# Kernel tuning notes

Hardware: AMD Instinct MI355X
Metric: run time of the kernel (lower is better)

## Reference

```python
import jax, jax.numpy as jnp
import numpy as np
import math

B, S, D, H = 2, 2048, 1024, 16
DK = D // H


def setup_inputs() -> dict:
    key = jax.random.key(0)
    ks = jax.random.split(key, 12)
    s = 0.02
    return {
        "query": jax.random.normal(ks[0], (B, S, D), jnp.float32),
        "key": jax.random.normal(ks[1], (B, S, D), jnp.float32),
        "value": jax.random.normal(ks[2], (B, S, D), jnp.float32),
        "mask": jnp.zeros((1, 1, S, S), jnp.float32),
        "Wq": jax.random.normal(ks[3], (D, D), jnp.float32) * s,
        "bq": jnp.zeros((D,), jnp.float32),
        "Wk": jax.random.normal(ks[4], (D, D), jnp.float32) * s,
        "bk": jnp.zeros((D,), jnp.float32),
        "Wv": jax.random.normal(ks[5], (D, D), jnp.float32) * s,
        "bv": jnp.zeros((D,), jnp.float32),
        "Wpost": jax.random.normal(ks[6], (D, D), jnp.float32) * s,
        "bpost": jnp.zeros((D,), jnp.float32),
        "per_dim_scale": jnp.zeros((DK,), jnp.float32),
    }


def reference(query, key, value, mask, Wq, bq, Wk, bk, Wv, bv, Wpost, bpost, per_dim_scale):
    # Linear projections (torch Linear: x @ W.T + b), split heads -> [B, H, S, DK]
    def proj(x, W, b):
        return (x @ W.T + b).reshape(B, S, H, DK).transpose(0, 2, 1, 3)

    q = proj(query, Wq, bq)
    k = proj(key, Wk, bk)
    v = proj(value, Wv, bv)

    # PerDimScale: scale = (1/ln2) / sqrt(d_k) * softplus(per_dim_scale)
    r_softplus_0 = 1.442695041
    scale = (r_softplus_0 / math.sqrt(DK)) * jax.nn.softplus(per_dim_scale)
    q = q * scale  # broadcast over last dim

    # Full attention matrix [B, H, S, S] + additive mask + softmax (dropout p=0)
    attn = jnp.einsum('bhqd,bhkd->bhqk', q, k) + mask
    attn = jax.nn.softmax(attn, axis=-1)

    out = jnp.einsum('bhqk,bhkd->bhqd', attn, v)
    out = out.transpose(0, 2, 1, 3).reshape(B, S, D)
    return out @ Wpost.T + bpost
```

## Files before the change

kernel.cpp:

```cpp
#include <hip/hip_runtime.h>
#include <math.h>

typedef __bf16 bf16;
typedef __bf16 bf16x8 __attribute__((ext_vector_type(8)));
typedef float f32x4 __attribute__((ext_vector_type(4)));

static constexpr int NB = 2, NS = 2048, ND = 1024, NH = 16, NDK = 64;
static constexpr float LOG2E = 1.442695041f;

__device__ __forceinline__ f32x4 mfma16(bf16x8 a, bf16x8 b, f32x4 c) {
  return __builtin_amdgcn_mfma_f32_16x16x32_bf16(a, b, c, 0, 0, 0);
}

__device__ __forceinline__ float exp2_fast(float x) {
  return __builtin_amdgcn_exp2f(x);
}

__device__ __forceinline__ void gload16(const void* g, void* l) {
  __builtin_amdgcn_global_load_lds(
      (const __attribute__((address_space(1))) void*)g,
      (__attribute__((address_space(3))) void*)l, 16, 0, 0);
}

__global__ void prep_kernel(const float* __restrict__ pds, float* __restrict__ scale,
                            const float* __restrict__ mask, int* __restrict__ flag, int n4) {
  if (blockIdx.x == 256) {
    int i = threadIdx.x;
    if (i < NDK) {
      float x = pds[i];
      float sp = fmaxf(x, 0.0f) + log1pf(expf(-fabsf(x)));
      scale[i] = (LOG2E * LOG2E / 8.0f) * sp;
    }
    return;
  }
  int idx = blockIdx.x * blockDim.x + threadIdx.x;
  int stride = 256 * blockDim.x;
  unsigned acc = 0;
  for (int i = idx; i < n4; i += stride) {
    float4 v = ((const float4*)mask)[i];
    acc |= (__float_as_uint(v.x) << 1) | (__float_as_uint(v.y) << 1)
         | (__float_as_uint(v.z) << 1) | (__float_as_uint(v.w) << 1);
  }
  if (acc != 0) atomicOr(flag, 1);
}

__global__ __launch_bounds__(256) void cvt_bf16(
    const float* __restrict__ s0, const float* __restrict__ s1, const float* __restrict__ s2,
    const float* __restrict__ s3, const float* __restrict__ s4, const float* __restrict__ s5,
    const float* __restrict__ s6,
    bf16* __restrict__ d0, bf16* __restrict__ d1, bf16* __restrict__ d2,
    bf16* __restrict__ d3, bf16* __restrict__ d4, bf16* __restrict__ d5,
    bf16* __restrict__ d6, int n8x, int n8w) {
  const int y = blockIdx.y;
  const float* s = y == 0 ? s0 : y == 1 ? s1 : y == 2 ? s2 : y == 3 ? s3
                 : y == 4 ? s4 : y == 5 ? s5 : s6;
  bf16* d = y == 0 ? d0 : y == 1 ? d1 : y == 2 ? d2 : y == 3 ? d3
          : y == 4 ? d4 : y == 5 ? d5 : d6;
  const int n8 = y < 3 ? n8x : n8w;
  for (int i = blockIdx.x * 256 + threadIdx.x; i < n8; i += gridDim.x * 256) {
    const float4* f = (const float4*)s + 2 * (size_t)i;
    float4 a = f[0], b = f[1];
    bf16x8 o;
    o[0] = (bf16)a.x; o[1] = (bf16)a.y; o[2] = (bf16)a.z; o[3] = (bf16)a.w;
    o[4] = (bf16)b.x; o[5] = (bf16)b.y; o[6] = (bf16)b.z; o[7] = (bf16)b.w;
    *((bf16x8*)d + i) = o;
  }
}

__global__ __launch_bounds__(256) void qkv_mm(
    const bf16* __restrict__ Xq, const bf16* __restrict__ Xk, const bf16* __restrict__ Xv,
    const bf16* __restrict__ Wqb, const bf16* __restrict__ Wkb, const bf16* __restrict__ Wvb,
    const float* __restrict__ bq, const float* __restrict__ bk, const float* __restrict__ bv,
    const float* __restrict__ scale2,
    bf16* __restrict__ Qs, bf16* __restrict__ Ks, bf16* __restrict__ Vt, int mode0) {
  __shared__ __align__(16) bf16 la[128 * 64];
  __shared__ __align__(16) bf16 lb[128 * 64];
  const int which = mode0 + blockIdx.y;
  const bf16* A  = which == 0 ? Xq  : which == 1 ? Xk  : Wvb;
  const bf16* Bm = which == 0 ? Wqb : which == 1 ? Wkb : Xv;
  const int t = threadIdx.x, lane = t & 63, wave = t >> 6;
  const int wm = wave >> 1, wn = wave & 1;
  int bm, bn;
  if (which == 2) { bm = blockIdx.x & 7; bn = blockIdx.x >> 3; }
  else            { bm = blockIdx.x >> 3; bn = blockIdx.x & 7; }
  const int g = lane >> 4, l15 = lane & 15;
  const int sr = wave * 8 + (lane >> 3);
  const int sc = ((lane & 7) ^ (lane >> 3)) * 8;
  const bf16* Abase = A  + (size_t)(bm * 128) * ND;
  const bf16* Bbase = Bm + (size_t)(bn * 128) * ND;

  f32x4 acc[4][4] = {};

  for (int kt = 0; kt < ND; kt += 64) {
    for (int c = 0; c < 4; ++c) {
      gload16(Abase + (size_t)(c * 32 + sr) * ND + kt + sc, la + c * 2048 + wave * 512);
      gload16(Bbase + (size_t)(c * 32 + sr) * ND + kt + sc, lb + c * 2048 + wave * 512);
    }
    __syncthreads();
    __builtin_amdgcn_s_setprio(1);
    for (int kk = 0; kk < 2; ++kk) {
      bf16x8 af[4], bfv[4];
      for (int m = 0; m < 4; ++m) {
        const int rr = wm * 64 + m * 16 + l15;
        af[m] = *(const bf16x8*)&la[rr * 64 + (((g + 4 * kk) ^ (rr & 7)) << 3)];
      }
      for (int n = 0; n < 4; ++n) {
        const int rr = wn * 64 + n * 16 + l15;
        bfv[n] = *(const bf16x8*)&lb[rr * 64 + (((g + 4 * kk) ^ (rr & 7)) << 3)];
      }
      for (int m = 0; m < 4; ++m)
        for (int n = 0; n < 4; ++n)
          acc[m][n] = mfma16(af[m], bfv[n], acc[m][n]);
    }
    __builtin_amdgcn_s_setprio(0);
    __syncthreads();
  }

  const int lr4 = g * 4;
  if (which != 2) {
    const float* bias = which ? bk : bq;
    bf16* outp = which ? Ks : Qs;
    for (int m = 0; m < 4; ++m) {
      const int grow0 = bm * 128 + wm * 64 + m * 16 + lr4;
      for (int n = 0; n < 4; ++n) {
        const int gcol = bn * 128 + wn * 64 + n * 16 + l15;
        const int h = gcol >> 6, dk = gcol & 63;
        const float bia = bias[gcol];
        const float sc2 = which ? 1.0f : scale2[dk];
        for (int r = 0; r < 4; ++r) {
          const int grow = grow0 + r;
          float v = acc[m][n][r] + bia;
          if (which == 0) v *= sc2;
          const int bb = grow >> 11, s = grow & (NS - 1);
          outp[(((size_t)(bb * NH + h)) * NS + s) * NDK + dk] = (bf16)v;
        }
      }
    }
  } else {
    for (int m = 0; m < 4; ++m) {
      const int d0 = bm * 128 + wm * 64 + m * 16 + lr4;
      for (int n = 0; n < 4; ++n) {
        const int gcol = bn * 128 + wn * 64 + n * 16 + l15;
        const int bb = gcol >> 11, s = gcol & (NS - 1);
        for (int r = 0; r < 4; ++r) {
          const int d = d0 + r;
          const float v = acc[m][n][r] + bv[d];
          const int h = d >> 6, dk = d & 63;
          Vt[(((size_t)(bb * NH + h)) * NDK + dk) * NS + s] = (bf16)v;
        }
      }
    }
  }
}

__global__ __launch_bounds__(256) void post_mm2(
    const bf16* __restrict__ A, const bf16* __restrict__ Bm,
    const float* __restrict__ bias, float* __restrict__ out) {
  __shared__ __align__(16) bf16 la[2][64 * 64];
  __shared__ __align__(16) bf16 lb[2][128 * 64];
  const int t = threadIdx.x, lane = t & 63, wave = t >> 6;
  const int bm = blockIdx.x >> 3, bn = blockIdx.x & 7;
  const int g = lane >> 4, l15 = lane & 15;
  const int sr = wave * 8 + (lane >> 3);
  const int sc = ((lane & 7) ^ (lane >> 3)) * 8;
  const bf16* Abase = A  + (size_t)(bm * 64) * ND;
  const bf16* Bbase = Bm + (size_t)(bn * 128) * ND;

  f32x4 acc[4][2] = {};

  auto stage = [&](int kt, int b) {
    for (int c = 0; c < 2; ++c)
      gload16(Abase + (size_t)(c * 32 + sr) * ND + kt + sc, la[b] + c * 2048 + wave * 512);
    for (int c = 0; c < 4; ++c)
      gload16(Bbase + (size_t)(c * 32 + sr) * ND + kt + sc, lb[b] + c * 2048 + wave * 512);
  };

  stage(0, 0);
  asm volatile("s_waitcnt vmcnt(0)" ::: "memory");
  __builtin_amdgcn_s_barrier();

  for (int it = 0; it < 16; ++it) {
    const int cur = it & 1;
    if (it + 1 < 16) stage((it + 1) * 64, cur ^ 1);

    __builtin_amdgcn_s_setprio(1);
    for (int kk = 0; kk < 2; ++kk) {
      bf16x8 af[4], bfv[2];
      for (int m = 0; m < 4; ++m) {
        const int rr = m * 16 + l15;
        af[m] = *(const bf16x8*)&la[cur][rr * 64 + (((g + 4 * kk) ^ (rr & 7)) << 3)];
      }
      for (int n = 0; n < 2; ++n) {
        const int rr = wave * 32 + n * 16 + l15;
        bfv[n] = *(const bf16x8*)&lb[cur][rr * 64 + (((g + 4 * kk) ^ (rr & 7)) << 3)];
      }
      for (int m = 0; m < 4; ++m)
        for (int n = 0; n < 2; ++n)
          acc[m][n] = mfma16(af[m], bfv[n], acc[m][n]);
    }
    __builtin_amdgcn_s_setprio(0);

    asm volatile("s_waitcnt vmcnt(0)" ::: "memory");
    __builtin_amdgcn_s_barrier();
  }

  for (int m = 0; m < 4; ++m) {
    const int grow0 = bm * 64 + m * 16 + g * 4;
    for (int n = 0; n < 2; ++n) {
      const int gcol = bn * 128 + wave * 32 + n * 16 + l15;
      const float bia = bias[gcol];
      for (int r = 0; r < 4; ++r)
        out[(size_t)(grow0 + r) * ND + gcol] = acc[m][n][r] + bia;
    }
  }
}

__global__ __launch_bounds__(512) void attn6(
    const bf16* __restrict__ Qs, const bf16* __restrict__ Ks,
    const bf16* __restrict__ Vt, const float* __restrict__ mask,
    const int* __restrict__ flag, bf16* __restrict__ Obs) {
  __shared__ __align__(16) bf16 lk[4 * 64 * 64];
  __shared__ __align__(16) bf16 lv[4 * 64 * 64];
  __shared__ __align__(16) bf16 lp[8 * 16 * 64];

  const int t = threadIdx.x, lane = t & 63, wave = t >> 6;
  const int g = lane >> 4, l15 = lane & 15;
  const int bh = blockIdx.y;
  const int qbase = blockIdx.x * 128 + wave * 16;
  const bool use_mask = (*flag) != 0;

  const bf16* Qh = Qs + (size_t)bh * NS * NDK;
  const bf16* Kh = Ks + (size_t)bh * NS * NDK;
  const bf16* Vh = Vt + (size_t)bh * NDK * NS;

  bf16x8 qf[2];
#pragma unroll
  for (int kk = 0; kk < 2; ++kk)
    qf[kk] = *(const bf16x8*)&Qh[(size_t)(qbase + l15) * NDK + kk * 32 + g * 8];

  f32x4 o_acc[4] = {};
  float lsum[4] = {0.0f, 0.0f, 0.0f, 0.0f};

  unsigned kfo[2][4];
#pragma unroll
  for (int kk = 0; kk < 2; ++kk)
#pragma unroll
    for (int n = 0; n < 4; ++n)
      kfo[kk][n] = (unsigned)((n * 16 + l15) * 64 + (((g + 4 * kk) ^ (l15 & 7)) << 3));
  unsigned pwo[4][4];
#pragma unroll
  for (int n = 0; n < 4; ++n)
#pragma unroll
    for (int r = 0; r < 4; ++r) {
      const int q = g * 4 + r;
      pwo[n][r] = (unsigned)(wave * 1024 + q * 64 + ((n * 16 + l15) ^ ((q & 7) << 3)));
    }
  unsigned pro[2];
#pragma unroll
  for (int kk = 0; kk < 2; ++kk)
    pro[kk] = (unsigned)(wave * 1024 + l15 * 64 + ((kk * 32 + g * 8) ^ ((l15 & 7) << 3)));

  const int srow = wave * 8 + (lane >> 3);
  const int sc = ((lane & 7) ^ (lane >> 3)) * 8;

  auto stage = [&](int kv, int b) {
    gload16(Kh + (size_t)(kv + srow) * NDK + sc, lk + b * 4096 + wave * 512);
    gload16(Vh + (size_t)srow * NS + kv + sc, lv + b * 4096 + wave * 512);
  };

  auto qkt = [&](int kv, int cur, f32x4 (&s)[4]) {
    __builtin_amdgcn_s_setprio(1);
#pragma unroll
    for (int kk = 0; kk < 2; ++kk)
#pragma unroll
      for (int n = 0; n < 4; ++n)
        s[n] = mfma16(qf[kk], *(const bf16x8*)&lk[cur * 4096 + kfo[kk][n]], s[n]);
    __builtin_amdgcn_s_setprio(0);
    if (use_mask) {
#pragma unroll
      for (int n = 0; n < 4; ++n)
#pragma unroll
        for (int r = 0; r < 4; ++r)
          s[n][r] += LOG2E * mask[(size_t)(qbase + g * 4 + r) * NS + kv + n * 16 + l15];
    }
  };

  auto expw = [&](f32x4 (&s)[4]) {
#pragma unroll
    for (int n = 0; n < 4; ++n)
#pragma unroll
      for (int r = 0; r < 4; ++r) {
        const float e = exp2_fast(s[n][r]);
        lsum[r] += e;
        lp[pwo[n][r]] = (bf16)e;
      }
  };

  auto pv = [&](int cur) {
#pragma unroll
    for (int kk = 0; kk < 2; ++kk) {
      const bf16x8 pf = *(const bf16x8*)&lp[pro[kk]];
      __builtin_amdgcn_s_setprio(1);
#pragma unroll
      for (int n = 0; n < 4; ++n)
        o_acc[n] = mfma16(pf, *(const bf16x8*)&lv[cur * 4096 + kfo[kk][n]], o_acc[n]);
      __builtin_amdgcn_s_setprio(0);
    }
  };

  auto pair = [&](int kv, int cA, int cB, int sA, int sB, bool doStage) {
    if (doStage) { stage(kv + 128, sA); stage(kv + 192, sB); }
    f32x4 sa[4] = {};
    qkt(kv, cA, sa);
    expw(sa);
    f32x4 sb[4] = {};
    qkt(kv + 64, cB, sb);
    pv(cA);
    expw(sb);
    pv(cB);
    asm volatile("s_waitcnt vmcnt(0)" ::: "memory");
    __builtin_amdgcn_s_barrier();
  };

  stage(0, 0);
  stage(64, 1);
  asm volatile("s_waitcnt vmcnt(0)" ::: "memory");
  __builtin_amdgcn_s_barrier();

  for (int p = 0; p < 16; p += 2) {
    pair(p * 128,       0, 1, 2, 3, true);
    pair(p * 128 + 128, 2, 3, 0, 1, p != 14);
  }

  const int bidx = bh >> 4, h = bh & 15;
#pragma unroll
  for (int r = 0; r < 4; ++r) {
    float rs = lsum[r];
    rs += __shfl_xor(rs, 1, 64);
    rs += __shfl_xor(rs, 2, 64);
    rs += __shfl_xor(rs, 4, 64);
    rs += __shfl_xor(rs, 8, 64);
    const float rinv = 1.0f / rs;
    const int qrow = qbase + g * 4 + r;
#pragma unroll
    for (int n = 0; n < 4; ++n)
      Obs[((size_t)(bidx * NS + qrow)) * ND + h * 64 + n * 16 + l15] = (bf16)(o_acc[n][r] * rinv);
  }
}

extern "C" void kernel_launch(void* const* d_in, const int* in_sizes, int n_in,
                              void* d_out, int out_size, void* d_ws, size_t ws_size,
                              hipStream_t stream) {
  (void)in_sizes; (void)n_in; (void)out_size;
  const float* query = (const float*)d_in[0];
  const float* key   = (const float*)d_in[1];
  const float* value = (const float*)d_in[2];
  const float* mask  = (const float*)d_in[3];
  const float* Wq    = (const float*)d_in[4];
  const float* bq    = (const float*)d_in[5];
  const float* Wk    = (const float*)d_in[6];
  const float* bk    = (const float*)d_in[7];
  const float* Wv    = (const float*)d_in[8];
  const float* bv    = (const float*)d_in[9];
  const float* Wpost = (const float*)d_in[10];
  const float* bpost = (const float*)d_in[11];
  const float* pds   = (const float*)d_in[12];

  char* ws = (char*)d_ws;
  const size_t MB = 1u << 20;
  bf16* Xq  = (bf16*)(ws + 0 * MB);
  bf16* Xk  = (bf16*)(ws + 8 * MB);
  bf16* Xv  = (bf16*)(ws + 16 * MB);
  bf16* Wqb = (bf16*)(ws + 24 * MB);
  bf16* Wkb = (bf16*)(ws + 26 * MB);
  bf16* Wvb = (bf16*)(ws + 28 * MB);
  bf16* Wpb = (bf16*)(ws + 30 * MB);
  float* scale2 = (float*)(ws + 32 * MB);
  int* flag     = (int*)(ws + 32 * MB + 256);

  const bool fused = ws_size >= (size_t)50 * MB;
  bf16 *Qsp, *Ksp, *Vtp, *Obsp;
  if (fused) {
    Qsp = (bf16*)d_out;
    Ksp = (bf16*)((char*)d_out + 8 * MB);
    Vtp = (bf16*)(ws + 33 * MB);
    Obsp = (bf16*)(ws + 41 * MB);
  } else {
    Qsp = (bf16*)d_out;
    Ksp = Xq;
    Vtp = Xk;
    Obsp = Xv;
  }

  (void)hipMemsetAsync(flag, 0, sizeof(int), stream);
  prep_kernel<<<257, 256, 0, stream>>>(pds, scale2, mask, flag, NS * NS / 4);

  cvt_bf16<<<dim3(256, 7), 256, 0, stream>>>(query, key, value, Wq, Wk, Wv, Wpost,
                                             Xq, Xk, Xv, Wqb, Wkb, Wvb, Wpb,
                                             NB * NS * ND / 8, ND * ND / 8);

  if (fused) {
    qkv_mm<<<dim3(256, 3), 256, 0, stream>>>(Xq, Xk, Xv, Wqb, Wkb, Wvb,
                                             bq, bk, bv, scale2, Qsp, Ksp, Vtp, 0);
  } else {
    qkv_mm<<<dim3(256, 1), 256, 0, stream>>>(Xq, Xk, Xv, Wqb, Wkb, Wvb,
                                             bq, bk, bv, scale2, Qsp, Ksp, Vtp, 0);
    qkv_mm<<<dim3(256, 1), 256, 0, stream>>>(Xq, Xk, Xv, Wqb, Wkb, Wvb,
                                             bq, bk, bv, scale2, Qsp, Ksp, Vtp, 1);
    qkv_mm<<<dim3(256, 1), 256, 0, stream>>>(Xq, Xk, Xv, Wqb, Wkb, Wvb,
                                             bq, bk, bv, scale2, Qsp, Ksp, Vtp, 2);
  }

  attn6<<<dim3(16, 32), 512, 0, stream>>>(Qsp, Ksp, Vtp, mask, flag, Obsp);

  post_mm2<<<512, 256, 0, stream>>>(Obsp, Wpb, bpost, (float*)d_out);
}
```

Baseline: 143.9 us.

## Give each attention wave two query tiles to reuse K/V fragments, halve block size

The attention kernel now uses 256-thread blocks in which each wave handles 32 query rows (two 16-row tiles) instead of 16. Each K and V fragment read from LDS feeds two MFMAs, which halves LDS reads per FLOP. The schedule also changes from four-buffer paired staging to simple double buffering with one 64-key tile per step. In exchange, register pressure rises and there are fewer waves per block to hide latency, and the shallower prefetch may expose more load latency.

```diff
diff --git a/kernel.cpp b/kernel.cpp
--- a/kernel.cpp
+++ b/kernel.cpp
@@ -215,31 +215,33 @@
   }
 }
 
-__global__ __launch_bounds__(512) void attn6(
+__global__ __launch_bounds__(256) void attn7(
     const bf16* __restrict__ Qs, const bf16* __restrict__ Ks,
     const bf16* __restrict__ Vt, const float* __restrict__ mask,
     const int* __restrict__ flag, bf16* __restrict__ Obs) {
-  __shared__ __align__(16) bf16 lk[4 * 64 * 64];
-  __shared__ __align__(16) bf16 lv[4 * 64 * 64];
-  __shared__ __align__(16) bf16 lp[8 * 16 * 64];
+  __shared__ __align__(16) bf16 lk[2 * 64 * 64];
+  __shared__ __align__(16) bf16 lv[2 * 64 * 64];
+  __shared__ __align__(16) bf16 lp[4 * 2 * 16 * 64];
 
   const int t = threadIdx.x, lane = t & 63, wave = t >> 6;
   const int g = lane >> 4, l15 = lane & 15;
   const int bh = blockIdx.y;
-  const int qbase = blockIdx.x * 128 + wave * 16;
+  const int qbase = blockIdx.x * 128 + wave * 32;
   const bool use_mask = (*flag) != 0;
 
   const bf16* Qh = Qs + (size_t)bh * NS * NDK;
   const bf16* Kh = Ks + (size_t)bh * NS * NDK;
   const bf16* Vh = Vt + (size_t)bh * NDK * NS;
 
-  bf16x8 qf[2];
-#pragma unroll
-  for (int kk = 0; kk < 2; ++kk)
-    qf[kk] = *(const bf16x8*)&Qh[(size_t)(qbase + l15) * NDK + kk * 32 + g * 8];
-
-  f32x4 o_acc[4] = {};
-  float lsum[4] = {0.0f, 0.0f, 0.0f, 0.0f};
+  bf16x8 qf[2][2];
+#pragma unroll
+  for (int mi = 0; mi < 2; ++mi)
+#pragma unroll
+    for (int kk = 0; kk < 2; ++kk)
+      qf[mi][kk] = *(const bf16x8*)&Qh[(size_t)(qbase + mi * 16 + l15) * NDK + kk * 32 + g * 8];
+
+  f32x4 o_acc[2][4] = {};
+  float lsum[2][4] = {};
 
   unsigned kfo[2][4];
 #pragma unroll
@@ -247,105 +249,116 @@
 #pragma unroll
     for (int n = 0; n < 4; ++n)
       kfo[kk][n] = (unsigned)((n * 16 + l15) * 64 + (((g + 4 * kk) ^ (l15 & 7)) << 3));
-  unsigned pwo[4][4];
-#pragma unroll
-  for (int n = 0; n < 4; ++n)
-#pragma unroll
-    for (int r = 0; r < 4; ++r) {
-      const int q = g * 4 + r;
-      pwo[n][r] = (unsigned)(wave * 1024 + q * 64 + ((n * 16 + l15) ^ ((q & 7) << 3)));
-    }
-  unsigned pro[2];
-#pragma unroll
-  for (int kk = 0; kk < 2; ++kk)
-    pro[kk] = (unsigned)(wave * 1024 + l15 * 64 + ((kk * 32 + g * 8) ^ ((l15 & 7) << 3)));
-
-  const int srow = wave * 8 + (lane >> 3);
+  unsigned pwo[2][4][4];
+#pragma unroll
+  for (int mi = 0; mi < 2; ++mi)
+#pragma unroll
+    for (int n = 0; n < 4; ++n)
+#pragma unroll
+      for (int r = 0; r < 4; ++r) {
+        const int q = g * 4 + r;
+        pwo[mi][n][r] = (unsigned)(wave * 2048 + mi * 1024 + q * 64 +
+                                   ((n * 16 + l15) ^ ((q & 7) << 3)));
+      }
+  unsigned pro[2][2];
+#pragma unroll
+  for (int mi = 0; mi < 2; ++mi)
+#pragma unroll
+    for (int kk = 0; kk < 2; ++kk)
+      pro[mi][kk] = (unsigned)(wave * 2048 + mi * 1024 + l15 * 64 +
+                               ((kk * 32 + g * 8) ^ ((l15 & 7) << 3)));
+
+  const int sr = wave * 8 + (lane >> 3);
   const int sc = ((lane & 7) ^ (lane >> 3)) * 8;
 
   auto stage = [&](int kv, int b) {
-    gload16(Kh + (size_t)(kv + srow) * NDK + sc, lk + b * 4096 + wave * 512);
-    gload16(Vh + (size_t)srow * NS + kv + sc, lv + b * 4096 + wave * 512);
+    for (int c = 0; c < 2; ++c) {
+      gload16(Kh + (size_t)(kv + c * 32 + sr) * NDK + sc, lk + b * 4096 + c * 2048 + wave * 512);
+      gload16(Vh + (size_t)(c * 32 + sr) * NS + kv + sc, lv + b * 4096 + c * 2048 + wave * 512);
+    }
   };
 
-  auto qkt = [&](int kv, int cur, f32x4 (&s)[4]) {
+  auto body = [&](int kv, int cur) {
+    if (kv + 64 < NS) stage(kv + 64, cur ^ 1);
+
+    f32x4 sa[2][4] = {};
     __builtin_amdgcn_s_setprio(1);
 #pragma unroll
     for (int kk = 0; kk < 2; ++kk)
 #pragma unroll
+      for (int n = 0; n < 4; ++n) {
+        const bf16x8 kf = *(const bf16x8*)&lk[cur * 4096 + kfo[kk][n]];
+        sa[0][n] = mfma16(qf[0][kk], kf, sa[0][n]);
+        sa[1][n] = mfma16(qf[1][kk], kf, sa[1][n]);
+      }
+    __builtin_amdgcn_s_setprio(0);
+
+    if (use_mask) {
+#pragma unroll
+      for (int mi = 0; mi < 2; ++mi)
+#pragma unroll
+        for (int n = 0; n < 4; ++n)
+#pragma unroll
+          for (int r = 0; r < 4; ++r)
+            sa[mi][n][r] += LOG2E *
+                mask[(size_t)(qbase + mi * 16 + g * 4 + r) * NS + kv + n * 16 + l15];
+    }
+
+#pragma unroll
+    for (int mi = 0; mi < 2; ++mi)
+#pragma unroll
       for (int n = 0; n < 4; ++n)
-        s[n] = mfma16(qf[kk], *(const bf16x8*)&lk[cur * 4096 + kfo[kk][n]], s[n]);
-    __builtin_amdgcn_s_setprio(0);
-    if (use_mask) {
-#pragma unroll
-      for (int n = 0; n < 4; ++n)
-#pragma unroll
-        for (int r = 0; r < 4; ++r)
-          s[n][r] += LOG2E * mask[(size_t)(qbase + g * 4 + r) * NS + kv + n * 16 + l15];
-    }
-  };
-
-  auto expw = [&](f32x4 (&s)[4]) {
-#pragma unroll
-    for (int n = 0; n < 4; ++n)
-#pragma unroll
-      for (int r = 0; r < 4; ++r) {
-        const float e = exp2_fast(s[n][r]);
-        lsum[r] += e;
-        lp[pwo[n][r]] = (bf16)e;
-      }
-  };
-
-  auto pv = [&](int cur) {
+#pragma unroll
+        for (int r = 0; r < 4; ++r) {
+          const float e = exp2_fast(sa[mi][n][r]);
+          lsum[mi][r] += e;
+          lp[pwo[mi][n][r]] = (bf16)e;
+        }
+
 #pragma unroll
     for (int kk = 0; kk < 2; ++kk) {
-      const bf16x8 pf = *(const bf16x8*)&lp[pro[kk]];
+      const bf16x8 pf0 = *(const bf16x8*)&lp[pro[0][kk]];
+      const bf16x8 pf1 = *(const bf16x8*)&lp[pro[1][kk]];
       __builtin_amdgcn_s_setprio(1);
 #pragma unroll
-      for (int n = 0; n < 4; ++n)
-        o_acc[n] = mfma16(pf, *(const bf16x8*)&lv[cur * 4096 + kfo[kk][n]], o_acc[n]);
+      for (int n = 0; n < 4; ++n) {
+        const bf16x8 vf = *(const bf16x8*)&lv[cur * 4096 + kfo[kk][n]];
+        o_acc[0][n] = mfma16(pf0, vf, o_acc[0][n]);
+        o_acc[1][n] = mfma16(pf1, vf, o_acc[1][n]);
+      }
       __builtin_amdgcn_s_setprio(0);
     }
-  };
-
-  auto pair = [&](int kv, int cA, int cB, int sA, int sB, bool doStage) {
-    if (doStage) { stage(kv + 128, sA); stage(kv + 192, sB); }
-    f32x4 sa[4] = {};
-    qkt(kv, cA, sa);
-    expw(sa);
-    f32x4 sb[4] = {};
-    qkt(kv + 64, cB, sb);
-    pv(cA);
-    expw(sb);
-    pv(cB);
+
     asm volatile("s_waitcnt vmcnt(0)" ::: "memory");
     __builtin_amdgcn_s_barrier();
   };
 
   stage(0, 0);
-  stage(64, 1);
   asm volatile("s_waitcnt vmcnt(0)" ::: "memory");
   __builtin_amdgcn_s_barrier();
 
-  for (int p = 0; p < 16; p += 2) {
-    pair(p * 128,       0, 1, 2, 3, true);
-    pair(p * 128 + 128, 2, 3, 0, 1, p != 14);
+  for (int kv = 0; kv < NS; kv += 128) {
+    body(kv, 0);
+    body(kv + 64, 1);
   }
 
   const int bidx = bh >> 4, h = bh & 15;
 #pragma unroll
-  for (int r = 0; r < 4; ++r) {
-    float rs = lsum[r];
-    rs += __shfl_xor(rs, 1, 64);
-    rs += __shfl_xor(rs, 2, 64);
-    rs += __shfl_xor(rs, 4, 64);
-    rs += __shfl_xor(rs, 8, 64);
-    const float rinv = 1.0f / rs;
-    const int qrow = qbase + g * 4 + r;
-#pragma unroll
-    for (int n = 0; n < 4; ++n)
-      Obs[((size_t)(bidx * NS + qrow)) * ND + h * 64 + n * 16 + l15] = (bf16)(o_acc[n][r] * rinv);
-  }
+  for (int mi = 0; mi < 2; ++mi)
+#pragma unroll
+    for (int r = 0; r < 4; ++r) {
+      float rs = lsum[mi][r];
+      rs += __shfl_xor(rs, 1, 64);
+      rs += __shfl_xor(rs, 2, 64);
+      rs += __shfl_xor(rs, 4, 64);
+      rs += __shfl_xor(rs, 8, 64);
+      const float rinv = 1.0f / rs;
+      const int qrow = qbase + mi * 16 + g * 4 + r;
+#pragma unroll
+      for (int n = 0; n < 4; ++n)
+        Obs[((size_t)(bidx * NS + qrow)) * ND + h * 64 + n * 16 + l15] =
+            (bf16)(o_acc[mi][n][r] * rinv);
+    }
 }
 
 extern "C" void kernel_launch(void* const* d_in, const int* in_sizes, int n_in,
@@ -411,7 +424,7 @@
                                              bq, bk, bv, scale2, Qsp, Ksp, Vtp, 2);
   }
 
-  attn6<<<dim3(16, 32), 512, 0, stream>>>(Qsp, Ksp, Vtp, mask, flag, Obsp);
+  attn7<<<dim3(16, 32), 256, 0, stream>>>(Qsp, Ksp, Vtp, mask, flag, Obsp);
 
   post_mm2<<<512, 256, 0, stream>>>(Obsp, Wpb, bpost, (float*)d_out);
 }
```

New measurement: 141.5 us. No clear change (-1.6%).

## Split attention KV range in halves with two query tiles per wave

Applied to the files above, without the earlier changes.

On the fused path, the attention kernel is replaced by attn8. Each wave now processes 32 query rows (two 16-row tiles) so every K and V fragment read from LDS feeds two MFMAs, and the key/value range is split across two blocks via blockIdx.z. The partial unnormalized outputs and row sums go to workspace, and a new combine kernel sums and normalizes them. This aims to halve LDS fragment traffic per MFMA and shorten each block's serial loop, at the cost of extra global traffic and a launch for the combine step. The older kernel is also simplified to a double-buffered single-tile loop and used only on the non-fused path.

```diff
diff --git a/kernel.cpp b/kernel.cpp
--- a/kernel.cpp
+++ b/kernel.cpp
@@ -215,12 +215,12 @@
   }
 }
 
-__global__ __launch_bounds__(512) void attn6(
+__global__ __launch_bounds__(512) void attn5(
     const bf16* __restrict__ Qs, const bf16* __restrict__ Ks,
     const bf16* __restrict__ Vt, const float* __restrict__ mask,
     const int* __restrict__ flag, bf16* __restrict__ Obs) {
-  __shared__ __align__(16) bf16 lk[4 * 64 * 64];
-  __shared__ __align__(16) bf16 lv[4 * 64 * 64];
+  __shared__ __align__(16) bf16 lk[2 * 64 * 64];
+  __shared__ __align__(16) bf16 lv[2 * 64 * 64];
   __shared__ __align__(16) bf16 lp[8 * 16 * 64];
 
   const int t = threadIdx.x, lane = t & 63, wave = t >> 6;
@@ -268,35 +268,35 @@
     gload16(Vh + (size_t)srow * NS + kv + sc, lv + b * 4096 + wave * 512);
   };
 
-  auto qkt = [&](int kv, int cur, f32x4 (&s)[4]) {
+  auto body = [&](int kv, int cur) {
+    if (kv + 64 < NS) stage(kv + 64, cur ^ 1);
+
+    f32x4 sacc[4] = {};
     __builtin_amdgcn_s_setprio(1);
 #pragma unroll
     for (int kk = 0; kk < 2; ++kk)
 #pragma unroll
       for (int n = 0; n < 4; ++n)
-        s[n] = mfma16(qf[kk], *(const bf16x8*)&lk[cur * 4096 + kfo[kk][n]], s[n]);
+        sacc[n] = mfma16(qf[kk], *(const bf16x8*)&lk[cur * 4096 + kfo[kk][n]], sacc[n]);
     __builtin_amdgcn_s_setprio(0);
+
     if (use_mask) {
 #pragma unroll
       for (int n = 0; n < 4; ++n)
 #pragma unroll
         for (int r = 0; r < 4; ++r)
-          s[n][r] += LOG2E * mask[(size_t)(qbase + g * 4 + r) * NS + kv + n * 16 + l15];
-    }
-  };
-
-  auto expw = [&](f32x4 (&s)[4]) {
+          sacc[n][r] += LOG2E * mask[(size_t)(qbase + g * 4 + r) * NS + kv + n * 16 + l15];
+    }
+
 #pragma unroll
     for (int n = 0; n < 4; ++n)
 #pragma unroll
       for (int r = 0; r < 4; ++r) {
-        const float e = exp2_fast(s[n][r]);
+        const float e = exp2_fast(sacc[n][r]);
         lsum[r] += e;
         lp[pwo[n][r]] = (bf16)e;
       }
-  };
-
-  auto pv = [&](int cur) {
+
 #pragma unroll
     for (int kk = 0; kk < 2; ++kk) {
       const bf16x8 pf = *(const bf16x8*)&lp[pro[kk]];
@@ -306,30 +306,18 @@
         o_acc[n] = mfma16(pf, *(const bf16x8*)&lv[cur * 4096 + kfo[kk][n]], o_acc[n]);
       __builtin_amdgcn_s_setprio(0);
     }
-  };
-
-  auto pair = [&](int kv, int cA, int cB, int sA, int sB, bool doStage) {
-    if (doStage) { stage(kv + 128, sA); stage(kv + 192, sB); }
-    f32x4 sa[4] = {};
-    qkt(kv, cA, sa);
-    expw(sa);
-    f32x4 sb[4] = {};
-    qkt(kv + 64, cB, sb);
-    pv(cA);
-    expw(sb);
-    pv(cB);
+
     asm volatile("s_waitcnt vmcnt(0)" ::: "memory");
     __builtin_amdgcn_s_barrier();
   };
 
   stage(0, 0);
-  stage(64, 1);
   asm volatile("s_waitcnt vmcnt(0)" ::: "memory");
   __builtin_amdgcn_s_barrier();
 
-  for (int p = 0; p < 16; p += 2) {
-    pair(p * 128,       0, 1, 2, 3, true);
-    pair(p * 128 + 128, 2, 3, 0, 1, p != 14);
+  for (int kv = 0; kv < NS; kv += 128) {
+    body(kv, 0);
+    body(kv + 64, 1);
   }
 
   const int bidx = bh >> 4, h = bh & 15;
@@ -345,6 +333,180 @@
 #pragma unroll
     for (int n = 0; n < 4; ++n)
       Obs[((size_t)(bidx * NS + qrow)) * ND + h * 64 + n * 16 + l15] = (bf16)(o_acc[n][r] * rinv);
+  }
+}
+
+__global__ __launch_bounds__(512, 4) void attn8(
+    const bf16* __restrict__ Qs, const bf16* __restrict__ Ks,
+    const bf16* __restrict__ Vt, const float* __restrict__ mask,
+    const int* __restrict__ flag,
+    bf16* __restrict__ O0, bf16* __restrict__ O1,
+    float* __restrict__ l0, float* __restrict__ l1) {
+  __shared__ __align__(16) bf16 lk[2 * 64 * 64];
+  __shared__ __align__(16) bf16 lv[2 * 64 * 64];
+  __shared__ __align__(16) bf16 lp[8 * 2 * 16 * 64];
+
+  const int t = threadIdx.x, lane = t & 63, wave = t >> 6;
+  const int g = lane >> 4, l15 = lane & 15;
+  const int bh = blockIdx.y;
+  const int half = blockIdx.z;
+  const int qbase = blockIdx.x * 256 + wave * 32;
+  const int kv0 = half * (NS / 2), kvEnd = kv0 + NS / 2;
+  const bool use_mask = (*flag) != 0;
+
+  const bf16* Qh = Qs + (size_t)bh * NS * NDK;
+  const bf16* Kh = Ks + (size_t)bh * NS * NDK;
+  const bf16* Vh = Vt + (size_t)bh * NDK * NS;
+
+  bf16x8 qf0[2], qf1[2];
+#pragma unroll
+  for (int kk = 0; kk < 2; ++kk) {
+    qf0[kk] = *(const bf16x8*)&Qh[(size_t)(qbase + l15) * NDK + kk * 32 + g * 8];
+    qf1[kk] = *(const bf16x8*)&Qh[(size_t)(qbase + 16 + l15) * NDK + kk * 32 + g * 8];
+  }
+
+  f32x4 o0[4] = {}, o1[4] = {};
+  float ls0[4] = {}, ls1[4] = {};
+
+  unsigned kfo[2][4];
+#pragma unroll
+  for (int kk = 0; kk < 2; ++kk)
+#pragma unroll
+    for (int n = 0; n < 4; ++n)
+      kfo[kk][n] = (unsigned)((n * 16 + l15) * 64 + (((g + 4 * kk) ^ (l15 & 7)) << 3));
+  unsigned pw0[4][4];
+#pragma unroll
+  for (int n = 0; n < 4; ++n)
+#pragma unroll
+    for (int r = 0; r < 4; ++r) {
+      const int q = g * 4 + r;
+      pw0[n][r] = (unsigned)(wave * 2048 + q * 64 + ((n * 16 + l15) ^ ((q & 7) << 3)));
+    }
+  unsigned pr0[2];
+#pragma unroll
+  for (int kk = 0; kk < 2; ++kk)
+    pr0[kk] = (unsigned)(wave * 2048 + l15 * 64 + ((kk * 32 + g * 8) ^ ((l15 & 7) << 3)));
+
+  const int srow = wave * 8 + (lane >> 3);
+  const int sc = ((lane & 7) ^ (lane >> 3)) * 8;
+
+  auto stage = [&](int kv, int b) {
+    gload16(Kh + (size_t)(kv + srow) * NDK + sc, lk + b * 4096 + wave * 512);
+    gload16(Vh + (size_t)srow * NS + kv + sc, lv + b * 4096 + wave * 512);
+  };
+
+  auto body = [&](int kv, int cur) {
+    if (kv + 64 < kvEnd) stage(kv + 64, cur ^ 1);
+
+    f32x4 sa0[4] = {}, sa1[4] = {};
+    __builtin_amdgcn_s_setprio(1);
+#pragma unroll
+    for (int kk = 0; kk < 2; ++kk)
+#pragma unroll
+      for (int n = 0; n < 4; ++n) {
+        const bf16x8 kf = *(const bf16x8*)&lk[cur * 4096 + kfo[kk][n]];
+        sa0[n] = mfma16(qf0[kk], kf, sa0[n]);
+        sa1[n] = mfma16(qf1[kk], kf, sa1[n]);
+      }
+    __builtin_amdgcn_s_setprio(0);
+
+    if (use_mask) {
+#pragma unroll
+      for (int n = 0; n < 4; ++n)
+#pragma unroll
+        for (int r = 0; r < 4; ++r) {
+          sa0[n][r] += LOG2E * mask[(size_t)(qbase + g * 4 + r) * NS + kv + n * 16 + l15];
+          sa1[n][r] += LOG2E * mask[(size_t)(qbase + 16 + g * 4 + r) * NS + kv + n * 16 + l15];
+        }
+    }
+
+#pragma unroll
+    for (int n = 0; n < 4; ++n)
+#pragma unroll
+      for (int r = 0; r < 4; ++r) {
+        const float e0 = exp2_fast(sa0[n][r]);
+        const float e1 = exp2_fast(sa1[n][r]);
+        ls0[r] += e0; ls1[r] += e1;
+        lp[pw0[n][r]] = (bf16)e0;
+        lp[pw0[n][r] + 1024] = (bf16)e1;
+      }
+
+#pragma unroll
+    for (int kk = 0; kk < 2; ++kk) {
+      const bf16x8 pf0 = *(const bf16x8*)&lp[pr0[kk]];
+      const bf16x8 pf1 = *(const bf16x8*)&lp[pr0[kk] + 1024];
+      __builtin_amdgcn_s_setprio(1);
+#pragma unroll
+      for (int n = 0; n < 4; ++n) {
+        const bf16x8 vf = *(const bf16x8*)&lv[cur * 4096 + kfo[kk][n]];
+        o0[n] = mfma16(pf0, vf, o0[n]);
+        o1[n] = mfma16(pf1, vf, o1[n]);
+      }
+      __builtin_amdgcn_s_setprio(0);
+    }
+
+    asm volatile("s_waitcnt vmcnt(0)" ::: "memory");
+    __builtin_amdgcn_s_barrier();
+  };
+
+  stage(kv0, 0);
+  asm volatile("s_waitcnt vmcnt(0)" ::: "memory");
+  __builtin_amdgcn_s_barrier();
+
+  for (int kv = kv0; kv < kvEnd; kv += 128) {
+    body(kv, 0);
+    body(kv + 64, 1);
+  }
+
+  bf16* Oh = half ? O1 : O0;
+  float* lh = half ? l1 : l0;
+  const int bidx = bh >> 4, h = bh & 15;
+#pragma unroll
+  for (int r = 0; r < 4; ++r) {
+    float rs = ls0[r];
+    rs += __shfl_xor(rs, 1, 64);
+    rs += __shfl_xor(rs, 2, 64);
+    rs += __shfl_xor(rs, 4, 64);
+    rs += __shfl_xor(rs, 8, 64);
+    const int qrow = qbase + g * 4 + r;
+    if (l15 == 0) lh[(size_t)bh * NS + qrow] = rs;
+#pragma unroll
+    for (int n = 0; n < 4; ++n)
+      Oh[((size_t)(bidx * NS + qrow)) * ND + h * 64 + n * 16 + l15] = (bf16)o0[n][r];
+  }
+#pragma unroll
+  for (int r = 0; r < 4; ++r) {
+    float rs = ls1[r];
+    rs += __shfl_xor(rs, 1, 64);
+    rs += __shfl_xor(rs, 2, 64);
+    rs += __shfl_xor(rs, 4, 64);
+    rs += __shfl_xor(rs, 8, 64);
+    const int qrow = qbase + 16 + g * 4 + r;
+    if (l15 == 0) lh[(size_t)bh * NS + qrow] = rs;
+#pragma unroll
+    for (int n = 0; n < 4; ++n)
+      Oh[((size_t)(bidx * NS + qrow)) * ND + h * 64 + n * 16 + l15] = (bf16)o1[n][r];
+  }
+}
+
+__global__ __launch_bounds__(256) void combine_kernel(
+    const bf16* __restrict__ O0, const bf16* __restrict__ O1,
+    const float* __restrict__ l0, const float* __restrict__ l1,
+    bf16* __restrict__ Obs) {
+  const int total = NB * NS * (ND / 8);
+  for (int i = blockIdx.x * 256 + threadIdx.x; i < total; i += gridDim.x * 256) {
+    const int row = i >> 7;
+    const int col = (i & 127) * 8;
+    const int bidx = row >> 11, qrow = row & (NS - 1), h = col >> 6;
+    const size_t li = (size_t)(bidx * NH + h) * NS + qrow;
+    const float rinv = 1.0f / (l0[li] + l1[li]);
+    const bf16x8 a = *((const bf16x8*)O0 + i);
+    const bf16x8 b = *((const bf16x8*)O1 + i);
+    bf16x8 o;
+#pragma unroll
+    for (int j = 0; j < 8; ++j)
+      o[j] = (bf16)(((float)a[j] + (float)b[j]) * rinv);
+    *((bf16x8*)Obs + i) = o;
   }
 }
 
@@ -402,6 +564,15 @@
   if (fused) {
     qkv_mm<<<dim3(256, 3), 256, 0, stream>>>(Xq, Xk, Xv, Wqb, Wkb, Wvb,
                                              bq, bk, bv, scale2, Qsp, Ksp, Vtp, 0);
+
+    bf16* O0p = (bf16*)(ws + 0 * MB);
+    bf16* O1p = (bf16*)(ws + 8 * MB);
+    float* l0p = (float*)(ws + 16 * MB);
+    float* l1p = (float*)(ws + 17 * MB);
+
+    attn8<<<dim3(8, 32, 2), 512, 0, stream>>>(Qsp, Ksp, Vtp, mask, flag,
+                                              O0p, O1p, l0p, l1p);
+    combine_kernel<<<1024, 256, 0, stream>>>(O0p, O1p, l0p, l1p, Obsp);
   } else {
     qkv_mm<<<dim3(256, 1), 256, 0, stream>>>(Xq, Xk, Xv, Wqb, Wkb, Wvb,
                                              bq, bk, bv, scale2, Qsp, Ksp, Vtp, 0);
@@ -409,9 +580,8 @@
                                              bq, bk, bv, scale2, Qsp, Ksp, Vtp, 1);
     qkv_mm<<<dim3(256, 1), 256, 0, stream>>>(Xq, Xk, Xv, Wqb, Wkb, Wvb,
                                              bq, bk, bv, scale2, Qsp, Ksp, Vtp, 2);
-  }
-
-  attn6<<<dim3(16, 32), 512, 0, stream>>>(Qsp, Ksp, Vtp, mask, flag, Obsp);
+    attn5<<<dim3(16, 32), 512, 0, stream>>>(Qsp, Ksp, Vtp, mask, flag, Obsp);
+  }
 
   post_mm2<<<512, 256, 0, stream>>>(Obsp, Wpb, bpost, (float*)d_out);
 }
```

Result: slower. 278.9 us (+93.9%).
